# Optimization experiments

Hardware: AMD Instinct MI355X
Metric: run time of the kernel (lower is better)

## Reference

```python
import jax, jax.numpy as jnp
import numpy as np
from jax import lax

NEG = -1e30  # log-space 'zero' that stays finite for stable grads


def _logadd3(a, b, c):
    m = jnp.maximum(jnp.maximum(a, b), c)
    return m + jnp.log(jnp.exp(a - m) + jnp.exp(b - m) + jnp.exp(c - m))


def _logadd2(a, b):
    m = jnp.maximum(a, b)
    return m + jnp.log(jnp.exp(a - m) + jnp.exp(b - m))


def setup_inputs() -> dict:
    key = jax.random.key(0)
    k1, k2, k3 = jax.random.split(key, 3)
    B, T, V, L = 64, 2000, 512, 200
    logits = jax.random.normal(k1, (B, T, V), dtype=jnp.float32)
    # keep input lengths well above 2*L+1 so all paths are feasible
    input_lengths = (T - jax.random.randint(k2, (B,), 0, 256)).astype(jnp.int32)
    targets = jax.random.randint(k3, (B, L), 0, V, dtype=jnp.int32)  # 0 == pad == blank
    return {"logits": logits, "input_lengths": input_lengths, "targets": targets}


def ctc_loss_sum(logits, input_lengths, targets):
    B, T, V = logits.shape
    L = targets.shape[1]
    S = 2 * L + 1

    lp = jax.nn.log_softmax(logits, axis=-1)  # [B,T,V]

    # compact nonzero targets per row (masked_select equivalent, fixed shape)
    mask = targets != 0
    tlen = mask.sum(-1)  # [B] target_lengths
    pos = jnp.where(mask, jnp.cumsum(mask, axis=1) - 1, L)
    compact = jnp.zeros_like(targets).at[jnp.arange(B)[:, None], pos].set(targets, mode="drop")

    # extended label sequence: blank, y1, blank, y2, ..., blank  -> [B,S]
    s_idx = jnp.arange(S)
    lab_idx = jnp.clip((s_idx - 1) // 2, 0, L - 1)
    ext = jnp.where(s_idx % 2 == 1, compact[:, lab_idx], 0)  # [B,S]

    # skip transition s-2 -> s allowed iff label at s is non-blank and differs from s-2
    ext_m2 = jnp.pad(ext, ((0, 0), (2, 0)))[:, :S]
    skip_ok = (ext != 0) & (ext != ext_m2) & (s_idx >= 2)  # [B,S]

    lpT = jnp.transpose(lp, (1, 0, 2))  # [T,B,V], scan over time

    # init: alpha_0[0]=lp(blank), alpha_0[1]=lp(y1)
    lp0_ext = jnp.take_along_axis(lpT[0], ext[:, :2], axis=1)  # [B,2]
    alpha0 = jnp.full((B, S), NEG, dtype=lp.dtype).at[:, :2].set(lp0_ext)

    def step(alpha, inp):
        lp_t, t = inp
        a1 = jnp.pad(alpha, ((0, 0), (1, 0)), constant_values=NEG)[:, :S]
        a2 = jnp.pad(alpha, ((0, 0), (2, 0)), constant_values=NEG)[:, :S]
        a2 = jnp.where(skip_ok, a2, NEG)
        lp_e = jnp.take_along_axis(lp_t, ext, axis=1)  # [B,S]
        new = _logadd3(alpha, a1, a2) + lp_e
        active = (t < input_lengths)[:, None]
        return jnp.where(active, new, alpha), None

    alphaT, _ = lax.scan(step, alpha0, (lpT[1:], jnp.arange(1, T)))

    # read out at final blank (2*tlen) and final label (2*tlen-1)
    e1 = (2 * tlen)[:, None]
    e2 = (2 * tlen - 1)
    a1 = jnp.take_along_axis(alphaT, e1, axis=1)[:, 0]
    a2 = jnp.where(e2 >= 0,
                   jnp.take_along_axis(alphaT, jnp.clip(e2, 0)[:, None], axis=1)[:, 0],
                   NEG)
    ll = _logadd2(a1, a2)  # [B] log p(targets | logits)
    return -jnp.sum(ll)


def reference(logits, input_lengths, targets):
    return ctc_loss_sum(logits, input_lengths, targets)
```

## Files before the change

kernel.cpp:

```cpp
#include <hip/hip_runtime.h>

#define B_ 64
#define T_ 2000
#define V_ 512
#define L_ 200
#define NJB 63


typedef _Float16 half4 __attribute__((ext_vector_type(4)));
union H4U { unsigned long long u; half4 h; float2 f2; };

__device__ __forceinline__ float dpp_shr1_f(float x) {
  return __int_as_float(__builtin_amdgcn_update_dpp(0, __float_as_int(x), 0x138, 0xf, 0xf, true));
}
__device__ __forceinline__ int dpp_shr1_i(int x) {
  return __builtin_amdgcn_update_dpp(0, x, 0x138, 0xf, 0xf, true);
}
__device__ __forceinline__ float dpp_shl1_f(float x) {
  return __int_as_float(__builtin_amdgcn_update_dpp(0, __float_as_int(x), 0x130, 0xf, 0xf, true));
}
__device__ __forceinline__ int dpp_shl1_i(int x) {
  return __builtin_amdgcn_update_dpp(0, x, 0x130, 0xf, 0xf, true);
}
#define DPPADD(v, ctrl, rmask)                                                              \
  v += __int_as_float(__builtin_amdgcn_update_dpp(0, __float_as_int(v), ctrl, rmask, 0xf, true));

#define COMPACT(BB)                                                          \
  int base = 0;                                                              \
  {                                                                          \
    cmp[lane] = 0; cmp[64 + lane] = 0; cmp[128 + lane] = 0; cmp[192 + lane] = 0; \
    _Pragma("unroll") for (int cc = 0; cc < 4; ++cc) {                       \
      const int l = cc * 64 + lane;                                          \
      const int v = (l < L_) ? targets[(BB) * L_ + l] : 0;                   \
      const unsigned long long mk = __ballot(v != 0);                        \
      const int pos = base + __popcll(mk & ((1ull << lane) - 1ull));         \
      if (v != 0) cmp[pos] = v;                                              \
      base += __popcll(mk);                                                  \
    }                                                                        \
    asm volatile("s_waitcnt lgkmcnt(0)" ::: "memory");                       \
  }

__global__ __launch_bounds__(256, 4) void kprob(const float* __restrict__ logits,
                                                const int* __restrict__ lens,
                                                const int* __restrict__ targets,
                                                unsigned long long* __restrict__ cull,
                                                float* __restrict__ bl) {
  const int tid = threadIdx.x;
  const int wid = tid >> 6;
  const int lane = tid & 63;
  __shared__ int cmp[256];
  __shared__ __align__(16) float scr[4][2][512];

  const int g = blockIdx.x;
  const int b = g & 63;
  const int jb = g >> 6;
  const int len = lens[b];
  const int nch = (len + 7) >> 3;
  if (wid == 0) { COMPACT(b); }
  __syncthreads();
  const int c = jb * 4 + wid;
  if (c >= nch) return;

  const int4 c4 = *(const int4*)(&cmp[4 * lane]);
  const int l0 = 4 * lane;
  const bool v0 = l0 + 0 < L_, v1 = l0 + 1 < L_, v2 = l0 + 2 < L_, v3 = l0 + 3 < L_;

  const float* rowp = logits + (size_t)b * (T_ * V_) + (size_t)c * (8 * V_);
  float4 X[16];
#pragma unroll
  for (int r = 0; r < 8; ++r) {
    X[2 * r] = *(const float4*)(rowp + r * V_ + 4 * lane);
    X[2 * r + 1] = *(const float4*)(rowp + r * V_ + 256 + 4 * lane);
  }
  const size_t obase = ((size_t)(b * T_ + c * 8)) * 64 + lane;
#pragma unroll
  for (int r = 0; r < 8; ++r) {
    const float4 xe = X[2 * r], xo = X[2 * r + 1];
    const float e0 = __expf(xe.x), e1 = __expf(xe.y), e2 = __expf(xe.z), e3 = __expf(xe.w);
    const float e4 = __expf(xo.x), e5 = __expf(xo.y), e6 = __expf(xo.z), e7 = __expf(xo.w);
    float s = ((e0 + e1) + (e2 + e3)) + ((e4 + e5) + (e6 + e7));
    DPPADD(s, 0x111, 0xf); DPPADD(s, 0x112, 0xf); DPPADD(s, 0x114, 0xf);
    DPPADD(s, 0x118, 0xf); DPPADD(s, 0x142, 0xa); DPPADD(s, 0x143, 0xc);
    const float sum = __int_as_float(__builtin_amdgcn_readlane(__float_as_int(s), 63));
    const float inv = 32.0f / sum;
    float* sc = &scr[wid][r & 1][0];
    *(float4*)(sc + 4 * lane) = make_float4(e0, e1, e2, e3);
    *(float4*)(sc + 256 + 4 * lane) = make_float4(e4, e5, e6, e7);
    asm volatile("s_waitcnt lgkmcnt(0)" ::: "memory");
    H4U p;
    p.h.x = (_Float16)(v0 ? sc[c4.x] * inv : 0.0f);
    p.h.y = (_Float16)(v1 ? sc[c4.y] * inv : 0.0f);
    p.h.z = (_Float16)(v2 ? sc[c4.z] * inv : 0.0f);
    p.h.w = (_Float16)(v3 ? sc[c4.w] * inv : 0.0f);
    cull[obase + (size_t)r * 64] = p.u;
    if (lane == 0) bl[b * 2048 + c * 8 + r] = e0 * inv;
  }
}

__global__ __launch_bounds__(64) void krec(const int* __restrict__ lens,
                                           const int* __restrict__ targets,
                                           const unsigned long long* __restrict__ cull,
                                           const float* __restrict__ bl,
                                           float* __restrict__ AF, int* __restrict__ EF,
                                           float* __restrict__ DD, int* __restrict__ EB) {
  const int lane = threadIdx.x;
  __shared__ int cmp[256];
  const int b = blockIdx.x >> 1;
  const int dirb = blockIdx.x & 1;
  const int len = lens[b];
  const int rem = len & 7;
  const int nch = (len + 7) >> 3;
  const int Cf = nch >> 1;
  const int Ntot = dirb ? (nch - Cf) : Cf;
  const int c0v = dirb ? (nch - 1) : 0;
  const int dstep = dirb ? -1 : 1;
#define CHK(J) (c0v + dstep * (J))

  COMPACT(b);
  const int tl = base;
  const int4 c4 = *(const int4*)(&cmp[4 * lane]);

  const int cm1 = __shfl_up(c4.w, 1);
  const float m0 = (lane > 0 && c4.x != 0 && c4.x != cm1) ? 1.0f : 0.0f;
  const float m1 = (c4.y != 0 && c4.y != c4.x) ? 1.0f : 0.0f;
  const float m2 = (c4.z != 0 && c4.z != c4.y) ? 1.0f : 0.0f;
  const float m3 = (c4.w != 0 && c4.w != c4.z) ? 1.0f : 0.0f;
  const float m0n = dpp_shl1_f(m0);

  float a0 = 0.f, a1 = 0.f, a2 = 0.f, a3 = 0.f, a4 = 0.f, a5 = 0.f, a6 = 0.f, a7 = 0.f;
  int E = 0;
  float fac = 1.0f;
  if (!dirb) {
    if (lane == 0) a0 = 1.0f;
  } else {
    const int st = 2 * tl;
    if (lane == (st >> 3)) {
      const int e = st & 7;
      a0 = (e == 0) ? 1.0f : 0.0f; a1 = (e == 1) ? 1.0f : 0.0f;
      a2 = (e == 2) ? 1.0f : 0.0f; a3 = (e == 3) ? 1.0f : 0.0f;
      a4 = (e == 4) ? 1.0f : 0.0f; a5 = (e == 5) ? 1.0f : 0.0f;
      a6 = (e == 6) ? 1.0f : 0.0f; a7 = (e == 7) ? 1.0f : 0.0f;
    }
  }

  unsigned long long LB0[8], LB1[8], LB2[8], LB3[8];
  float4 BLa0, BLb0, BLa1, BLb1, BLa2, BLb2, BLa3, BLb3;

#define LOADC(S, CIDX)                                                       \
  {                                                                          \
    const int c_ = (CIDX);                                                   \
    const unsigned long long* pp_ = cull + ((size_t)(b * T_ + c_ * 8)) * 64 + lane; \
    _Pragma("unroll") for (int u = 0; u < 8; ++u) LB##S[u] = pp_[(size_t)u * 64]; \
    const float* bf_ = bl + b * 2048 + c_ * 8;                               \
    BLa##S = *(const float4*)(bf_);                                          \
    BLb##S = *(const float4*)(bf_ + 4);                                      \
  }

#define PREFETCH(S)                                                          \
  {                                                                          \
    const int nx_ = i + 4;                                                   \
    if (nx_ < Ntot) LOADC(S, CHK(nx_));                                      \
  }

#define STEP8F(S)                                                            \
  {                                                                          \
    const float blv_[8] = {BLa##S.x, BLa##S.y, BLa##S.z, BLa##S.w,           \
                           BLb##S.x, BLb##S.y, BLb##S.z, BLb##S.w};          \
    _Pragma("unroll") for (int u = 0; u < 8; ++u) {                          \
      H4U q_; q_.u = LB##S[u];                                               \
      const float qx = (float)q_.h.x, qy = (float)q_.h.y;                    \
      const float qz = (float)q_.h.z, qw = (float)q_.h.w;                    \
      const float pbv = blv_[u];                                             \
      const float s1 = dpp_shr1_f(a7) * fac;                 \
      float n0 = (a0 + s1) * pbv;                                            \
      float n1 = fmaf(m0, s1, a0 + a1) * qx;                                 \
      float n2 = (a2 + a1) * pbv;                                            \
      float n3 = fmaf(m1, a1, a2 + a3) * qy;                                 \
      float n4 = (a4 + a3) * pbv;                                            \
      float n5 = fmaf(m2, a3, a4 + a5) * qz;                                 \
      float n6 = (a6 + a5) * pbv;                                            \
      float n7 = fmaf(m3, a5, a6 + a7) * qw;                                 \
      a0 = n0; a1 = n1; a2 = n2; a3 = n3;                                    \
      a4 = n4; a5 = n5; a6 = n6; a7 = n7;                                    \
    }                                                                        \
  }

#define STEP8B(S, UHI)                                                       \
  {                                                                          \
    const float blv_[8] = {BLa##S.x, BLa##S.y, BLa##S.z, BLa##S.w,           \
                           BLb##S.x, BLb##S.y, BLb##S.z, BLb##S.w};          \
    _Pragma("unroll") for (int u = 7; u >= 0; --u) {                         \
      if (u <= (UHI)) {                                                      \
        H4U q_; q_.u = LB##S[u];                                             \
        const float qx = (float)q_.h.x, qy = (float)q_.h.y;                  \
        const float qz = (float)q_.h.z, qw = (float)q_.h.w;                  \
        const float pbv = blv_[u];                                           \
        const float sa = dpp_shl1_f(a0) * fac;              \
        const float sb = dpp_shl1_f(a1) * fac;                               \
        float n0 = (a0 + a1) * pbv;                                          \
        float n1 = fmaf(m1, a3, a1 + a2) * qx;                               \
        float n2 = (a2 + a3) * pbv;                                          \
        float n3 = fmaf(m2, a5, a3 + a4) * qy;                               \
        float n4 = (a4 + a5) * pbv;                                          \
        float n5 = fmaf(m3, a7, a5 + a6) * qz;                               \
        float n6 = (a6 + a7) * pbv;                                          \
        float n7 = fmaf(m0n, sb, a7 + sa) * qw;                              \
        a0 = n0; a1 = n1; a2 = n2; a3 = n3;                                  \
        a4 = n4; a5 = n5; a6 = n6; a7 = n7;                                  \
      }                                                                      \
    }                                                                        \
  }

#define RENORM_COMMON                                                        \
    const float mx = fmaxf(fmaxf(fmaxf(a0, a1), fmaxf(a2, a3)),              \
                           fmaxf(fmaxf(a4, a5), fmaxf(a6, a7)));             \
    const bool dead = (mx == 0.0f);                                          \
    int e_ = (int)((__float_as_uint(mx) >> 23) & 0xff) - 127;                \
    if (dead) e_ = 0;                                                        \
    const float sc_ = __int_as_float((unsigned)(127 - e_) << 23);            \
    a0 *= sc_; a1 *= sc_; a2 *= sc_; a3 *= sc_;                              \
    a4 *= sc_; a5 *= sc_; a6 *= sc_; a7 *= sc_;                              \
    const int En_ = E + e_;

#define RENORMF                                                              \
  {                                                                          \
    RENORM_COMMON                                                            \
    const int EnP_ = dpp_shr1_i(En_);                                        \
    E = dead ? EnP_ : En_;                                                   \
    const int Ep_ = dpp_shr1_i(E);                                           \
    const int d_ = Ep_ - E;                                                  \
    int dc_ = d_ < -126 ? -126 : (d_ > 126 ? 126 : d_);                      \
    fac = (d_ < -126) ? 0.0f : __int_as_float((unsigned)(dc_ + 127) << 23);  \
  }

#define RENORMB                                                              \
  {                                                                          \
    RENORM_COMMON                                                            \
    const int EnP_ = dpp_shl1_i(En_);                                        \
    E = dead ? EnP_ : En_;                                                   \
    const int Ep_ = dpp_shl1_i(E);                                           \
    const int d_ = Ep_ - E;                                                  \
    int dc_ = d_ < -126 ? -126 : (d_ > 126 ? 126 : d_);                      \
    fac = (d_ < -126) ? 0.0f : __int_as_float((unsigned)(dc_ + 127) << 23);  \
  }

  LOADC(0, CHK(0)); LOADC(1, CHK(1)); LOADC(2, CHK(2)); LOADC(3, CHK(3));

  if (!dirb) {
    for (int i = 0; i < Ntot; ++i) {
      switch (i & 3) {
        case 0: STEP8F(0); RENORMF; PREFETCH(0); break;
        case 1: STEP8F(1); RENORMF; PREFETCH(1); break;
        case 2: STEP8F(2); RENORMF; PREFETCH(2); break;
        default: STEP8F(3); RENORMF; PREFETCH(3); break;
      }
    }
    *(float4*)(AF + b * 512 + lane * 8) = make_float4(a0, a1, a2, a3);
    *(float4*)(AF + b * 512 + lane * 8 + 4) = make_float4(a4, a5, a6, a7);
    EF[b * 64 + lane] = E;
  } else {
    for (int i = 0; i < Ntot; ++i) {
      const int uh = (i == 0 && rem) ? (rem - 1) : 7;
      switch (i & 3) {
        case 0: STEP8B(0, uh); RENORMB; PREFETCH(0); break;
        case 1: STEP8B(1, uh); RENORMB; PREFETCH(1); break;
        case 2: STEP8B(2, uh); RENORMB; PREFETCH(2); break;
        default: STEP8B(3, uh); RENORMB; PREFETCH(3); break;
      }
    }
    const float sa = dpp_shl1_f(a0) * fac;
    const float sb = dpp_shl1_f(a1) * fac;
    const float d0 = a0 + a1;
    const float d1 = fmaf(m1, a3, a1 + a2);
    const float d2 = a2 + a3;
    const float d3 = fmaf(m2, a5, a3 + a4);
    const float d4 = a4 + a5;
    const float d5 = fmaf(m3, a7, a5 + a6);
    const float d6 = a6 + a7;
    const float d7 = fmaf(m0n, sb, a7 + sa);
    *(float4*)(DD + b * 512 + lane * 8) = make_float4(d0, d1, d2, d3);
    *(float4*)(DD + b * 512 + lane * 8 + 4) = make_float4(d4, d5, d6, d7);
    EB[b * 64 + lane] = E;
  }
#undef LOADC
#undef PREFETCH
#undef STEP8F
#undef STEP8B
#undef RENORM_COMMON
#undef RENORMF
#undef RENORMB
#undef CHK
}

__global__ __launch_bounds__(512) void kcomb(const int* __restrict__ lens,
                                             const float* __restrict__ AF,
                                             const int* __restrict__ EF,
                                             const float* __restrict__ DD,
                                             const int* __restrict__ EB,
                                             float* __restrict__ out) {
  const int wid = threadIdx.x >> 6;
  const int lane = threadIdx.x & 63;
  __shared__ float part[8];
  float acc = 0.0f;
#pragma unroll
  for (int q = 0; q < 8; ++q) {
    const int b = wid * 8 + q;
    const float4 f0 = *(const float4*)(AF + b * 512 + lane * 8);
    const float4 f1 = *(const float4*)(AF + b * 512 + lane * 8 + 4);
    const float4 g0 = *(const float4*)(DD + b * 512 + lane * 8);
    const float4 g1 = *(const float4*)(DD + b * 512 + lane * 8 + 4);
    const float dot = ((f0.x * g0.x + f0.y * g0.y) + (f0.z * g0.z + f0.w * g0.w)) +
                      ((f1.x * g1.x + f1.y * g1.y) + (f1.z * g1.z + f1.w * g1.w));
    const int Es = EF[b * 64 + lane] + EB[b * 64 + lane];
    const bool z = (dot == 0.0f);
    int Ek = z ? (-(1 << 28)) : Es;
#pragma unroll
    for (int off = 32; off; off >>= 1) {
      const int o = __shfl_xor(Ek, off);
      Ek = o > Ek ? o : Ek;
    }
    float v = z ? 0.0f : ldexpf(dot, Es - Ek);
#pragma unroll
    for (int off = 32; off; off >>= 1) v += __shfl_xor(v, off);
    const float ll = __logf(v) + (float)Ek * 0.69314718056f - (float)lens[b] * 3.46573590280f;
    acc -= ll;
  }
  if (lane == 0) part[wid] = acc;
  __syncthreads();
  if (threadIdx.x == 0) {
    float s = ((part[0] + part[1]) + (part[2] + part[3])) +
              ((part[4] + part[5]) + (part[6] + part[7]));
    out[0] = s;
  }
}

extern "C" void kernel_launch(void* const* d_in, const int* in_sizes, int n_in,
                              void* d_out, int out_size, void* d_ws, size_t ws_size,
                              hipStream_t stream) {
  const float* logits = (const float*)d_in[0];
  const int* input_lengths = (const int*)d_in[1];
  const int* targets = (const int*)d_in[2];
  float* out = (float*)d_out;
  unsigned long long* cull = (unsigned long long*)d_ws;
  float* bl = (float*)((char*)d_ws + 65536000);
  float* AF = (float*)((char*)d_ws + 66125824);
  int* EF = (int*)((char*)d_ws + 66256896);
  float* DD = (float*)((char*)d_ws + 66273280);
  int* EB = (int*)((char*)d_ws + 66404352);
  (void)in_sizes; (void)n_in; (void)out_size; (void)ws_size;

  kprob<<<B_ * NJB, 256, 0, stream>>>(logits, input_lengths, targets, cull, bl);
  krec<<<2 * B_, 64, 0, stream>>>(input_lengths, targets, cull, bl, AF, EF, DD, EB);
  kcomb<<<1, 512, 0, stream>>>(input_lengths, AF, EF, DD, EB, out);
}
```

Before: 479.3 us.

## Pack per-step probabilities into 16-byte chunks, nontemporal stores, deeper recurrence prefetch

The producer kernel now interleaves pairs of timesteps so each lane writes one 16-byte vector, using nontemporal stores. The blank probabilities are batched into two vector stores from lane 0 instead of eight scalar stores. The recurrence kernel reads the new layout with four 128-bit loads per chunk instead of eight 64-bit loads, and its software prefetch ring grows from 4 to 6 chunks to hide more latency on its serial critical path. The cost is higher register pressure in the single-wave recurrence kernel, and the nontemporal hint may keep the intermediate buffer out of cache before the consumer reads it.

```diff
diff --git a/kernel.cpp b/kernel.cpp
--- a/kernel.cpp
+++ b/kernel.cpp
@@ -5,10 +5,14 @@
 #define V_ 512
 #define L_ 200
 #define NJB 63
+#define NCH 250
 
 
 typedef _Float16 half4 __attribute__((ext_vector_type(4)));
-union H4U { unsigned long long u; half4 h; float2 f2; };
+typedef unsigned long long ull;
+typedef ull u64x2 __attribute__((ext_vector_type(2)));
+typedef float f32x4 __attribute__((ext_vector_type(4)));
+union H4U { unsigned long long u; half4 h; };
 
 __device__ __forceinline__ float dpp_shr1_f(float x) {
   return __int_as_float(__builtin_amdgcn_update_dpp(0, __float_as_int(x), 0x138, 0xf, 0xf, true));
@@ -43,7 +47,7 @@
 __global__ __launch_bounds__(256, 4) void kprob(const float* __restrict__ logits,
                                                 const int* __restrict__ lens,
                                                 const int* __restrict__ targets,
-                                                unsigned long long* __restrict__ cull,
+                                                u64x2* __restrict__ cull2,
                                                 float* __restrict__ bl) {
   const int tid = threadIdx.x;
   const int wid = tid >> 6;
@@ -72,7 +76,9 @@
     X[2 * r] = *(const float4*)(rowp + r * V_ + 4 * lane);
     X[2 * r + 1] = *(const float4*)(rowp + r * V_ + 256 + 4 * lane);
   }
-  const size_t obase = ((size_t)(b * T_ + c * 8)) * 64 + lane;
+  u64x2* outp = cull2 + ((size_t)(b * NCH + c) * 4) * 64 + lane;
+  unsigned long long pe = 0;
+  float blb0 = 0, blb1 = 0, blb2 = 0, blb3 = 0, blb4 = 0, blb5 = 0, blb6 = 0, blb7 = 0;
 #pragma unroll
   for (int r = 0; r < 8; ++r) {
     const float4 xe = X[2 * r], xo = X[2 * r + 1];
@@ -92,14 +98,32 @@
     p.h.y = (_Float16)(v1 ? sc[c4.y] * inv : 0.0f);
     p.h.z = (_Float16)(v2 ? sc[c4.z] * inv : 0.0f);
     p.h.w = (_Float16)(v3 ? sc[c4.w] * inv : 0.0f);
-    cull[obase + (size_t)r * 64] = p.u;
-    if (lane == 0) bl[b * 2048 + c * 8 + r] = e0 * inv;
+    if (r & 1) {
+      u64x2 w; w.x = pe; w.y = p.u;
+      __builtin_nontemporal_store(w, outp + (r >> 1) * 64);
+    } else {
+      pe = p.u;
+    }
+    const float bv = e0 * inv;
+    switch (r) {
+      case 0: blb0 = bv; break; case 1: blb1 = bv; break;
+      case 2: blb2 = bv; break; case 3: blb3 = bv; break;
+      case 4: blb4 = bv; break; case 5: blb5 = bv; break;
+      case 6: blb6 = bv; break; default: blb7 = bv; break;
+    }
+  }
+  if (lane == 0) {
+    f32x4* bp = (f32x4*)(bl + b * 2048 + c * 8);
+    f32x4 w0 = {blb0, blb1, blb2, blb3};
+    f32x4 w1 = {blb4, blb5, blb6, blb7};
+    __builtin_nontemporal_store(w0, bp);
+    __builtin_nontemporal_store(w1, bp + 1);
   }
 }
 
 __global__ __launch_bounds__(64) void krec(const int* __restrict__ lens,
                                            const int* __restrict__ targets,
-                                           const unsigned long long* __restrict__ cull,
+                                           const u64x2* __restrict__ cull2,
                                            const float* __restrict__ bl,
                                            float* __restrict__ AF, int* __restrict__ EF,
                                            float* __restrict__ DD, int* __restrict__ EB) {
@@ -143,31 +167,28 @@
     }
   }
 
-  unsigned long long LB0[8], LB1[8], LB2[8], LB3[8];
-  float4 BLa0, BLb0, BLa1, BLb1, BLa2, BLb2, BLa3, BLb3;
+  u64x2 Qa0, Qb0, Qc0, Qd0, Qa1, Qb1, Qc1, Qd1, Qa2, Qb2, Qc2, Qd2;
+  u64x2 Qa3, Qb3, Qc3, Qd3, Qa4, Qb4, Qc4, Qd4, Qa5, Qb5, Qc5, Qd5;
+  float4 BLa0, BLb0, BLa1, BLb1, BLa2, BLb2, BLa3, BLb3, BLa4, BLb4, BLa5, BLb5;
 
 #define LOADC(S, CIDX)                                                       \
   {                                                                          \
     const int c_ = (CIDX);                                                   \
-    const unsigned long long* pp_ = cull + ((size_t)(b * T_ + c_ * 8)) * 64 + lane; \
-    _Pragma("unroll") for (int u = 0; u < 8; ++u) LB##S[u] = pp_[(size_t)u * 64]; \
+    const u64x2* pp_ = cull2 + ((size_t)(b * NCH + c_) * 4) * 64 + lane;     \
+    Qa##S = pp_[0]; Qb##S = pp_[64]; Qc##S = pp_[128]; Qd##S = pp_[192];     \
     const float* bf_ = bl + b * 2048 + c_ * 8;                               \
     BLa##S = *(const float4*)(bf_);                                          \
     BLb##S = *(const float4*)(bf_ + 4);                                      \
   }
 
-#define PREFETCH(S)                                                          \
-  {                                                                          \
-    const int nx_ = i + 4;                                                   \
-    if (nx_ < Ntot) LOADC(S, CHK(nx_));                                      \
-  }
-
 #define STEP8F(S)                                                            \
   {                                                                          \
     const float blv_[8] = {BLa##S.x, BLa##S.y, BLa##S.z, BLa##S.w,           \
                            BLb##S.x, BLb##S.y, BLb##S.z, BLb##S.w};          \
+    const unsigned long long qu_[8] = {Qa##S.x, Qa##S.y, Qb##S.x, Qb##S.y,   \
+                                       Qc##S.x, Qc##S.y, Qd##S.x, Qd##S.y};  \
     _Pragma("unroll") for (int u = 0; u < 8; ++u) {                          \
-      H4U q_; q_.u = LB##S[u];                                               \
+      H4U q_; q_.u = qu_[u];                                                 \
       const float qx = (float)q_.h.x, qy = (float)q_.h.y;                    \
       const float qz = (float)q_.h.z, qw = (float)q_.h.w;                    \
       const float pbv = blv_[u];                                             \
@@ -189,9 +210,11 @@
   {                                                                          \
     const float blv_[8] = {BLa##S.x, BLa##S.y, BLa##S.z, BLa##S.w,           \
                            BLb##S.x, BLb##S.y, BLb##S.z, BLb##S.w};          \
+    const unsigned long long qu_[8] = {Qa##S.x, Qa##S.y, Qb##S.x, Qb##S.y,   \
+                                       Qc##S.x, Qc##S.y, Qd##S.x, Qd##S.y};  \
     _Pragma("unroll") for (int u = 7; u >= 0; --u) {                         \
       if (u <= (UHI)) {                                                      \
-        H4U q_; q_.u = LB##S[u];                                             \
+        H4U q_; q_.u = qu_[u];                                               \
         const float qx = (float)q_.h.x, qy = (float)q_.h.y;                  \
         const float qz = (float)q_.h.z, qw = (float)q_.h.w;                  \
         const float pbv = blv_[u];                                           \
@@ -244,29 +267,42 @@
     fac = (d_ < -126) ? 0.0f : __int_as_float((unsigned)(dc_ + 127) << 23);  \
   }
 
-  LOADC(0, CHK(0)); LOADC(1, CHK(1)); LOADC(2, CHK(2)); LOADC(3, CHK(3));
+  LOADC(0, CHK(0)); LOADC(1, CHK(1)); LOADC(2, CHK(2));
+  LOADC(3, CHK(3)); LOADC(4, CHK(4)); LOADC(5, CHK(5));
 
   if (!dirb) {
+    int ph = 0;
     for (int i = 0; i < Ntot; ++i) {
-      switch (i & 3) {
-        case 0: STEP8F(0); RENORMF; PREFETCH(0); break;
-        case 1: STEP8F(1); RENORMF; PREFETCH(1); break;
-        case 2: STEP8F(2); RENORMF; PREFETCH(2); break;
-        default: STEP8F(3); RENORMF; PREFETCH(3); break;
+      const int nx = i + 6;
+      const bool pf = nx < Ntot;
+      switch (ph) {
+        case 0: STEP8F(0); RENORMF; if (pf) LOADC(0, CHK(nx)); break;
+        case 1: STEP8F(1); RENORMF; if (pf) LOADC(1, CHK(nx)); break;
+        case 2: STEP8F(2); RENORMF; if (pf) LOADC(2, CHK(nx)); break;
+        case 3: STEP8F(3); RENORMF; if (pf) LOADC(3, CHK(nx)); break;
+        case 4: STEP8F(4); RENORMF; if (pf) LOADC(4, CHK(nx)); break;
+        default: STEP8F(5); RENORMF; if (pf) LOADC(5, CHK(nx)); break;
       }
+      ph = (ph == 5) ? 0 : ph + 1;
     }
     *(float4*)(AF + b * 512 + lane * 8) = make_float4(a0, a1, a2, a3);
     *(float4*)(AF + b * 512 + lane * 8 + 4) = make_float4(a4, a5, a6, a7);
     EF[b * 64 + lane] = E;
   } else {
+    int ph = 0;
     for (int i = 0; i < Ntot; ++i) {
+      const int nx = i + 6;
+      const bool pf = nx < Ntot;
       const int uh = (i == 0 && rem) ? (rem - 1) : 7;
-      switch (i & 3) {
-        case 0: STEP8B(0, uh); RENORMB; PREFETCH(0); break;
-        case 1: STEP8B(1, uh); RENORMB; PREFETCH(1); break;
-        case 2: STEP8B(2, uh); RENORMB; PREFETCH(2); break;
-        default: STEP8B(3, uh); RENORMB; PREFETCH(3); break;
+      switch (ph) {
+        case 0: STEP8B(0, uh); RENORMB; if (pf) LOADC(0, CHK(nx)); break;
+        case 1: STEP8B(1, uh); RENORMB; if (pf) LOADC(1, CHK(nx)); break;
+        case 2: STEP8B(2, uh); RENORMB; if (pf) LOADC(2, CHK(nx)); break;
+        case 3: STEP8B(3, uh); RENORMB; if (pf) LOADC(3, CHK(nx)); break;
+        case 4: STEP8B(4, uh); RENORMB; if (pf) LOADC(4, CHK(nx)); break;
+        default: STEP8B(5, uh); RENORMB; if (pf) LOADC(5, CHK(nx)); break;
       }
+      ph = (ph == 5) ? 0 : ph + 1;
     }
     const float sa = dpp_shl1_f(a0) * fac;
     const float sb = dpp_shl1_f(a1) * fac;
@@ -283,7 +319,6 @@
     EB[b * 64 + lane] = E;
   }
 #undef LOADC
-#undef PREFETCH
 #undef STEP8F
 #undef STEP8B
 #undef RENORM_COMMON
@@ -341,7 +376,7 @@
   const int* input_lengths = (const int*)d_in[1];
   const int* targets = (const int*)d_in[2];
   float* out = (float*)d_out;
-  unsigned long long* cull = (unsigned long long*)d_ws;
+  u64x2* cull2 = (u64x2*)d_ws;
   float* bl = (float*)((char*)d_ws + 65536000);
   float* AF = (float*)((char*)d_ws + 66125824);
   int* EF = (int*)((char*)d_ws + 66256896);
@@ -349,7 +384,7 @@
   int* EB = (int*)((char*)d_ws + 66404352);
   (void)in_sizes; (void)n_in; (void)out_size; (void)ws_size;
 
-  kprob<<<B_ * NJB, 256, 0, stream>>>(logits, input_lengths, targets, cull, bl);
-  krec<<<2 * B_, 64, 0, stream>>>(input_lengths, targets, cull, bl, AF, EF, DD, EB);
+  kprob<<<B_ * NJB, 256, 0, stream>>>(logits, input_lengths, targets, cull2, bl);
+  krec<<<2 * B_, 64, 0, stream>>>(input_lengths, targets, cull2, bl, AF, EF, DD, EB);
   kcomb<<<1, 512, 0, stream>>>(input_lengths, AF, EF, DD, EB, out);
 }
```

After: 559.4 us. 16.7% more time.
